# Kernel tuning notes

Hardware: AMD Instinct MI355X
Metric: run time of the kernel (lower is better)

Reference implementation:

```python
import jax, jax.numpy as jnp
import numpy as np

TOUT = 4096  # fixed padded output frame length (>= max possible cumsum of durations)


def setup_inputs() -> dict:
    key = jax.random.key(0)
    k1, k2 = jax.random.split(key)
    xs = jax.random.normal(k1, (8, 512, 384), dtype=jnp.float32)
    ds = jax.random.randint(k2, (8, 512), 0, 8, dtype=jnp.int64)
    return {"xs": xs, "ds": ds}


def reference(xs, ds):
    # xs: (B, Tin, D) phoneme embeddings; ds: (B, Tin) integer durations.
    # Build mapping matrix M: (B, Tout, Tin) where M[b, t, i] = 1 iff frame t
    # falls in [cumsum(ds)[i] - ds[i], cumsum(ds)[i]), then ys = M @ xs.
    cum = jnp.cumsum(ds, axis=1)          # (B, Tin) right boundaries
    left = cum - ds                        # (B, Tin) left boundaries
    frames = jnp.arange(TOUT)              # (Tout,)
    f = frames[None, :, None]              # (1, Tout, 1)
    M = ((f >= left[:, None, :]) & (f < cum[:, None, :])).astype(xs.dtype)  # (B, Tout, Tin)
    ys = jnp.einsum('bti,bid->btd', M, xs)  # (B, Tout, D)
    return ys
```

## Files before the change

### kernel.cpp

```cpp
#include <hip/hip_runtime.h>

#define NB    8
#define NIN   512
#define TOUT  4096
#define ND    384
#define J4    (ND / 4)
#define TROWS 16
#define BLK   256

typedef float f32x4 __attribute__((ext_vector_type(4)));

__global__ __launch_bounds__(BLK) void lenreg(const f32x4* __restrict__ xs,
                                              const int* __restrict__ ds,
                                              f32x4* __restrict__ out) {
    const int b       = blockIdx.x & 7;
    const int rowbase = (blockIdx.x >> 3) * TROWS;
    const int tid     = threadIdx.x;

    __shared__ int cum[NIN];
    __shared__ int wsum[BLK / 64];
    __shared__ int owner[TROWS];

    const int* dsb = ds + b * NIN;
    const int a0 = dsb[2 * tid];
    const int a1 = dsb[2 * tid + 1];
    int p = a0 + a1;
    const int lane = tid & 63;
    const int wid  = tid >> 6;
    #pragma unroll
    for (int off = 1; off < 64; off <<= 1) {
        int v = __shfl_up(p, off, 64);
        if (lane >= off) p += v;
    }
    if (lane == 63) wsum[wid] = p;
    __syncthreads();
    int acc = 0;
    #pragma unroll
    for (int w = 0; w < BLK / 64; ++w)
        if (w < wid) acc += wsum[w];
    p += acc;
    cum[2 * tid + 1] = p;
    cum[2 * tid]     = p - a1;
    __syncthreads();

    const int total = cum[NIN - 1];
    if (tid < TROWS) {
        const int t = rowbase + tid;
        int o = -1;
        if (t < total) {
            int lo = 0, hi = NIN;
            #pragma unroll
            for (int s = 0; s < 10; ++s) {
                if (lo < hi) {
                    int mid = (lo + hi) >> 1;
                    if (cum[mid] > t) hi = mid; else lo = mid + 1;
                }
            }
            o = lo;
        }
        owner[tid] = o;
    }
    __syncthreads();

    const f32x4* xsb  = xs + (size_t)b * NIN * J4;
    f32x4*       outb = out + ((size_t)b * TOUT + rowbase) * J4;
    constexpr int ITER = TROWS * J4 / BLK;
    f32x4 v[ITER];
    #pragma unroll
    for (int k = 0; k < ITER; ++k) {
        const int g = k * BLK + tid;
        const int o = owner[g / J4];
        v[k] = (f32x4)(0.f);
        if (o >= 0) v[k] = xsb[o * J4 + (g - (g / J4) * J4)];
    }
    #pragma unroll
    for (int k = 0; k < ITER; ++k)
        outb[k * BLK + tid] = v[k];
}

extern "C" void kernel_launch(void* const* d_in, const int* in_sizes, int n_in,
                              void* d_out, int out_size, void* d_ws, size_t ws_size,
                              hipStream_t stream) {
    const float* xs = (const float*)d_in[0];
    const int*   ds = (const int*)d_in[1];
    float* out = (float*)d_out;

    lenreg<<<(TOUT / TROWS) * NB, BLK, 0, stream>>>((const f32x4*)xs, ds,
                                                    (f32x4*)out);
}
```

Baseline: 74.08 us.

## Precompute frame-owner table in a separate kernel instead of per-block scan

The fused kernel is split in two. A small kernel runs once per batch: it does the prefix sum of durations and scatters each phoneme index into a global owner table of TOUT entries per batch, initialised to -1. The gather kernel then reads owner indices from that table instead of every block redoing the 512-element scan and binary search. This removes redundant per-block scan work and barriers, at the cost of an extra kernel launch and a small round trip through global workspace.

```diff
diff --git a/kernel.cpp b/kernel.cpp
--- a/kernel.cpp
+++ b/kernel.cpp
@@ -10,21 +10,14 @@
 
 typedef float f32x4 __attribute__((ext_vector_type(4)));
 
-__global__ __launch_bounds__(BLK) void lenreg(const f32x4* __restrict__ xs,
-                                              const int* __restrict__ ds,
-                                              f32x4* __restrict__ out) {
-    const int b       = blockIdx.x & 7;
-    const int rowbase = (blockIdx.x >> 3) * TROWS;
-    const int tid     = threadIdx.x;
+__global__ __launch_bounds__(NIN) void build_owner(const int* __restrict__ ds,
+                                                   int* __restrict__ owner) {
+    const int b   = blockIdx.x;
+    const int tid = threadIdx.x;
+    __shared__ int wsum[NIN / 64];
 
-    __shared__ int cum[NIN];
-    __shared__ int wsum[BLK / 64];
-    __shared__ int owner[TROWS];
-
-    const int* dsb = ds + b * NIN;
-    const int a0 = dsb[2 * tid];
-    const int a1 = dsb[2 * tid + 1];
-    int p = a0 + a1;
+    const int d = ds[b * NIN + tid];
+    int p = d;
     const int lane = tid & 63;
     const int wid  = tid >> 6;
     #pragma unroll
@@ -33,45 +26,44 @@
         if (lane >= off) p += v;
     }
     if (lane == 63) wsum[wid] = p;
+
+    int* ob = owner + b * TOUT;
+    #pragma unroll
+    for (int t = tid; t < TOUT; t += NIN) ob[t] = -1;
     __syncthreads();
+
     int acc = 0;
     #pragma unroll
-    for (int w = 0; w < BLK / 64; ++w)
+    for (int w = 0; w < NIN / 64; ++w)
         if (w < wid) acc += wsum[w];
     p += acc;
-    cum[2 * tid + 1] = p;
-    cum[2 * tid]     = p - a1;
-    __syncthreads();
+    int right = p < TOUT ? p : TOUT;
+    for (int t = p - d; t < right; ++t) ob[t] = tid;
+}
 
-    const int total = cum[NIN - 1];
-    if (tid < TROWS) {
-        const int t = rowbase + tid;
-        int o = -1;
-        if (t < total) {
-            int lo = 0, hi = NIN;
-            #pragma unroll
-            for (int s = 0; s < 10; ++s) {
-                if (lo < hi) {
-                    int mid = (lo + hi) >> 1;
-                    if (cum[mid] > t) hi = mid; else lo = mid + 1;
-                }
-            }
-            o = lo;
-        }
-        owner[tid] = o;
-    }
-    __syncthreads();
+__global__ __launch_bounds__(BLK) void gather(const f32x4* __restrict__ xs,
+                                              const int* __restrict__ owner,
+                                              f32x4* __restrict__ out) {
+    const int b       = blockIdx.x & 7;
+    const int rowbase = (blockIdx.x >> 3) * TROWS;
+    const int tid     = threadIdx.x;
 
+    const int*   ob   = owner + b * TOUT + rowbase;
     const f32x4* xsb  = xs + (size_t)b * NIN * J4;
     f32x4*       outb = out + ((size_t)b * TOUT + rowbase) * J4;
+
     constexpr int ITER = TROWS * J4 / BLK;
+    int   o[ITER];
     f32x4 v[ITER];
+    #pragma unroll
+    for (int k = 0; k < ITER; ++k)
+        o[k] = ob[(k * BLK + tid) / J4];
     #pragma unroll
     for (int k = 0; k < ITER; ++k) {
         const int g = k * BLK + tid;
-        const int o = owner[g / J4];
+        const int j = g - (g / J4) * J4;
         v[k] = (f32x4)(0.f);
-        if (o >= 0) v[k] = xsb[o * J4 + (g - (g / J4) * J4)];
+        if (o[k] >= 0) v[k] = xsb[o[k] * J4 + j];
     }
     #pragma unroll
     for (int k = 0; k < ITER; ++k)
@@ -84,7 +76,9 @@
     const float* xs = (const float*)d_in[0];
     const int*   ds = (const int*)d_in[1];
     float* out = (float*)d_out;
+    int* owner = (int*)d_ws;
 
-    lenreg<<<(TOUT / TROWS) * NB, BLK, 0, stream>>>((const f32x4*)xs, ds,
+    build_owner<<<NB, NIN, 0, stream>>>(ds, owner);
+    gather<<<(TOUT / TROWS) * NB, BLK, 0, stream>>>((const f32x4*)xs, owner,
                                                     (f32x4*)out);
 }
```

After: 76.83 us. 3.7% more time.
